# Kernel optimization log

Hardware: AMD Instinct MI355X
Metric: run time of the kernel (lower is better)

Reference implementation:

```python
import jax, jax.numpy as jnp
import numpy as np

EMBED_DIM = 1024
WINDOW = 256
NUM_HEADS = 16
HEAD_DIM = EMBED_DIM // NUM_HEADS
SCALE = HEAD_DIM ** (-0.5)


def setup_inputs() -> dict:
    key = jax.random.key(0)
    ks = jax.random.split(key, 9)
    B, S, E = 4, 4096, EMBED_DIM
    std = E ** (-0.5)
    x = jax.random.normal(ks[0], (B, S, E), dtype=jnp.float32)
    Wq = jax.random.normal(ks[1], (E, E), dtype=jnp.float32) * std
    Wk = jax.random.normal(ks[2], (E, E), dtype=jnp.float32) * std
    Wv = jax.random.normal(ks[3], (E, E), dtype=jnp.float32) * std
    Wo = jax.random.normal(ks[4], (E, E), dtype=jnp.float32) * std
    bq = jax.random.normal(ks[5], (E,), dtype=jnp.float32) * 0.01
    bk = jax.random.normal(ks[6], (E,), dtype=jnp.float32) * 0.01
    bv = jax.random.normal(ks[7], (E,), dtype=jnp.float32) * 0.01
    bo = jax.random.normal(ks[8], (E,), dtype=jnp.float32) * 0.01
    return {"x": x, "Wq": Wq, "bq": bq, "Wk": Wk, "bk": bk,
            "Wv": Wv, "bv": bv, "Wo": Wo, "bo": bo}


def reference(x, Wq, bq, Wk, bk, Wv, bv, Wo, bo):
    B, S, E = x.shape
    W = WINDOW
    nw = S // W  # seq_len chosen divisible by window_size
    # projections (torch Linear: x @ W.T + b); no head split in the original
    q = x @ Wq.T + bq
    k = x @ Wk.T + bk
    v = x @ Wv.T + bv
    # split into non-overlapping windows: [B, nw, W, E]
    qw = q.reshape(B, nw, W, E)
    kw = k.reshape(B, nw, W, E)
    vw = v.reshape(B, nw, W, E)
    scores = jnp.einsum('bnqe,bnke->bnqk', qw, kw) * SCALE  # [B, nw, W, W]
    causal = jnp.tril(jnp.ones((W, W), dtype=bool))
    scores = jnp.where(causal, scores, -jnp.inf)
    attn = jax.nn.softmax(scores, axis=-1)
    out = jnp.einsum('bnqk,bnke->bnqe', attn, vw).reshape(B, S, E)
    out = out @ Wo.T + bo
    return out + x
```

## Files before the change

### kernel.cpp

```cpp
#include <hip/hip_runtime.h>
#include <hip/hip_bf16.h>


typedef unsigned short u16;
typedef __attribute__((ext_vector_type(8))) short short8;
typedef __attribute__((ext_vector_type(4))) short short4v;
typedef __attribute__((ext_vector_type(4))) float f32x4;

__device__ __forceinline__ u16 f2bf(float f) {
    __hip_bfloat16 h = __float2bfloat16(f);
    return __builtin_bit_cast(u16, h);
}

__global__ void cast_f32_bf16(const float* __restrict__ src, u16* __restrict__ dst, int n) {
    int i = (blockIdx.x * 256 + threadIdx.x) * 8;
    if (i >= n) return;
    const float4* s = (const float4*)(src + i);
    float4 a = s[0], b = s[1];
    short8 o;
    o[0] = (short)f2bf(a.x); o[1] = (short)f2bf(a.y); o[2] = (short)f2bf(a.z); o[3] = (short)f2bf(a.w);
    o[4] = (short)f2bf(b.x); o[5] = (short)f2bf(b.y); o[6] = (short)f2bf(b.z); o[7] = (short)f2bf(b.w);
    *(short8*)(dst + i) = o;
}

__global__ void wcast(const float* __restrict__ Wq, const float* __restrict__ Wk,
                      const float* __restrict__ Wv, const float* __restrict__ Wo,
                      u16* __restrict__ WqT, u16* __restrict__ WkT,
                      u16* __restrict__ WvT, u16* __restrict__ Wob)
{
    __shared__ float lt[64][65];
    const int which = blockIdx.x >> 8;
    const int bid = blockIdx.x & 255;
    const int c0 = (bid & 15) * 64, r0 = (bid >> 4) * 64;
    const int t = threadIdx.x;
    const int tr = t >> 3, tc = (t & 7) * 8;
    const float* src = which == 0 ? Wq : which == 1 ? Wk : which == 2 ? Wv : Wo;
    if (which == 3) {
#pragma unroll
        for (int p = 0; p < 2; ++p) {
            int r = p * 32 + tr;
            const float* s = src + (size_t)(r0 + r) * 1024 + c0 + tc;
            float4 a = *(const float4*)s, b = *(const float4*)(s + 4);
            short8 o;
            o[0] = (short)f2bf(a.x); o[1] = (short)f2bf(a.y); o[2] = (short)f2bf(a.z); o[3] = (short)f2bf(a.w);
            o[4] = (short)f2bf(b.x); o[5] = (short)f2bf(b.y); o[6] = (short)f2bf(b.z); o[7] = (short)f2bf(b.w);
            *(short8*)(Wob + (size_t)(r0 + r) * 1024 + c0 + tc) = o;
        }
        return;
    }
    u16* dst = which == 0 ? WqT : which == 1 ? WkT : WvT;
#pragma unroll
    for (int p = 0; p < 2; ++p) {
        int r = p * 32 + tr;
        const float* s = src + (size_t)(r0 + r) * 1024 + c0 + tc;
        float4 a = *(const float4*)s, b = *(const float4*)(s + 4);
        lt[r][tc + 0] = a.x; lt[r][tc + 1] = a.y; lt[r][tc + 2] = a.z; lt[r][tc + 3] = a.w;
        lt[r][tc + 4] = b.x; lt[r][tc + 5] = b.y; lt[r][tc + 6] = b.z; lt[r][tc + 7] = b.w;
    }
    __syncthreads();
#pragma unroll
    for (int p = 0; p < 2; ++p) {
        int r = p * 32 + tr;
        short8 o;
#pragma unroll
        for (int j = 0; j < 8; ++j) o[j] = (short)f2bf(lt[tc + j][r]);
        *(short8*)(dst + (size_t)(c0 + r) * 1024 + r0 + tc) = o;
    }
}

__global__ void ub2(const float* __restrict__ Wk, const float* __restrict__ bq,
                    const float* __restrict__ Wo, const float* __restrict__ bv,
                    const float* __restrict__ bo, float* __restrict__ u, float* __restrict__ b2)
{
    const int t = threadIdx.x, bid = blockIdx.x;
    if (bid < 4) {
        int b = bid * 256 + t;
        float acc = 0.f;
        for (int o = 0; o < 1024; ++o) acc += Wk[(size_t)o * 1024 + b] * bq[o];
        u[b] = acc;
    } else {
        int n = (bid - 4) * 16 + (t >> 4);
        int l = t & 15;
        float acc = 0.f;
        for (int m = l; m < 1024; m += 16) acc += Wo[(size_t)n * 1024 + m] * bv[m];
#pragma unroll
        for (int s = 1; s < 16; s <<= 1) acc += __shfl_xor(acc, s, 64);
        if (l == 0) b2[n] = acc + bo[n];
    }
}

__global__ __launch_bounds__(256, 4) void gemm_small_dual(
    const u16* __restrict__ HA, const u16* __restrict__ HB, u16* __restrict__ HC,
    const u16* __restrict__ WA, const u16* __restrict__ WB, u16* __restrict__ WC)
{
    __shared__ __align__(16) u16 At[64 * 64], Bt[64 * 64];
    const bool sec = blockIdx.x >= 256;
    const u16* A = sec ? WA : HA;
    const u16* B = sec ? WB : HB;
    u16* C = sec ? WC : HC;
    const int bid = blockIdx.x & 255;
    const int m0 = (bid >> 4) * 64, n0 = (bid & 15) * 64;
    const int t = threadIdx.x, lane = t & 63, w = t >> 6;
    const int l15 = lane & 15, lk = lane >> 4;

    f32x4 acc[4];
#pragma unroll
    for (int m = 0; m < 4; ++m) acc[m] = (f32x4){0.f, 0.f, 0.f, 0.f};

    for (int k0 = 0; k0 < 1024; k0 += 64) {
        __syncthreads();
#pragma unroll
        for (int p = 0; p < 2; ++p) {
            int e = p * 2048 + t * 8;
            int row = e >> 6, col = e & 63;
            short8 va = *(const short8*)(A + (size_t)(m0 + row) * 1024 + k0 + col);
            *(short8*)((char*)At + row * 128 + ((col * 2) ^ ((row & 7) << 4))) = va;
            short8 vb = *(const short8*)(B + (size_t)(n0 + row) * 1024 + k0 + col);
            *(short8*)((char*)Bt + row * 128 + ((col * 2) ^ ((row & 7) << 4))) = vb;
        }
        __syncthreads();
#pragma unroll
        for (int ks = 0; ks < 2; ++ks) {
            int bc = ks * 64 + lk * 16;
            int brow = w * 16 + l15;
            short8 bfr = *(const short8*)((char*)Bt + brow * 128 + (bc ^ ((brow & 7) << 4)));
#pragma unroll
            for (int m = 0; m < 4; ++m) {
                int arow = m * 16 + l15;
                short8 af = *(const short8*)((char*)At + arow * 128 + (bc ^ ((arow & 7) << 4)));
                acc[m] = __builtin_amdgcn_mfma_f32_16x16x32_bf16(af, bfr, acc[m], 0, 0, 0);
            }
        }
    }
#pragma unroll
    for (int m = 0; m < 4; ++m)
#pragma unroll
        for (int r = 0; r < 4; ++r) {
            int row = m0 + m * 16 + lk * 4 + r;
            int col = n0 + w * 16 + l15;
            C[(size_t)row * 1024 + col] = f2bf(acc[m][r]);
        }
}

__global__ __launch_bounds__(256, 2) void gemm_yv(
    const u16* __restrict__ A, const u16* __restrict__ BH, const u16* __restrict__ BW,
    const float* __restrict__ ub, u16* __restrict__ Y, u16* __restrict__ V2t)
{
    __shared__ __align__(16) u16 At[128 * 64];
    __shared__ __align__(16) u16 Bt[128 * 64];
    const int t = threadIdx.x;
    const int lane = t & 63;
    const int wid = t >> 6;
    const int wm = wid >> 1, wn = wid & 1;
    const int l15 = lane & 15, lk = lane >> 4;
    const int K = 1024;

    const int bid = blockIdx.y * gridDim.x + blockIdx.x;
    const int cpx = 2048 >> 3;
    const int swz = (bid & 7) * cpx + (bid >> 3);
    const int tn = swz & 15;
    const int tm = swz >> 4;
    const int m0 = tm * 128;
    const bool isv = tn >= 8;
    const int n0 = (tn & 7) * 128;
    const u16* B = isv ? BW : BH;

    f32x4 acc[4][4];
#pragma unroll
    for (int m = 0; m < 4; ++m)
#pragma unroll
        for (int n = 0; n < 4; ++n)
            acc[m][n] = (f32x4){0.f, 0.f, 0.f, 0.f};

    for (int k0 = 0; k0 < K; k0 += 64) {
        __syncthreads();
#pragma unroll
        for (int p = 0; p < 4; ++p) {
            int e = p * 2048 + t * 8;
            int row = e >> 6, col = e & 63;
            short8 va = *(const short8*)(A + (size_t)(m0 + row) * K + k0 + col);
            *(short8*)((char*)At + row * 128 + ((col * 2) ^ ((row & 7) << 4))) = va;
            short8 vb = *(const short8*)(B + (size_t)(n0 + row) * K + k0 + col);
            *(short8*)((char*)Bt + row * 128 + ((col * 2) ^ ((row & 7) << 4))) = vb;
        }
        __syncthreads();
#pragma unroll
        for (int ks = 0; ks < 2; ++ks) {
            const int bc = ks * 64 + lk * 16;
            short8 af[4], bfr[4];
#pragma unroll
            for (int m = 0; m < 4; ++m) {
                int row = wm * 64 + m * 16 + l15;
                af[m] = *(const short8*)((char*)At + row * 128 + (bc ^ ((row & 7) << 4)));
            }
#pragma unroll
            for (int n = 0; n < 4; ++n) {
                int row = wn * 64 + n * 16 + l15;
                bfr[n] = *(const short8*)((char*)Bt + row * 128 + (bc ^ ((row & 7) << 4)));
            }
#pragma unroll
            for (int m = 0; m < 4; ++m)
#pragma unroll
                for (int n = 0; n < 4; ++n)
                    acc[m][n] = __builtin_amdgcn_mfma_f32_16x16x32_bf16(af[m], bfr[n], acc[m][n], 0, 0, 0);
        }
    }

    if (!isv) {
#pragma unroll
        for (int m = 0; m < 4; ++m)
#pragma unroll
            for (int n = 0; n < 4; ++n) {
                int col = n0 + wn * 64 + n * 16 + l15;
                float bv = ub[col];
#pragma unroll
                for (int r = 0; r < 4; ++r) {
                    int row = m0 + wm * 64 + m * 16 + lk * 4 + r;
                    Y[(size_t)row * 1024 + col] = f2bf(acc[m][n][r] + bv);
                }
            }
    } else {
#pragma unroll
        for (int m = 0; m < 4; ++m)
#pragma unroll
            for (int n = 0; n < 4; ++n) {
                int col = n0 + wn * 64 + n * 16 + l15;
                int row0 = m0 + wm * 64 + m * 16 + lk * 4;
                short4v pk;
#pragma unroll
                for (int r = 0; r < 4; ++r) pk[r] = (short)f2bf(acc[m][n][r]);
                *(short4v*)(V2t + (size_t)col * 16384 + row0) = pk;
            }
    }
}

__global__ __launch_bounds__(256, 2) void attn_win(
    const u16* __restrict__ y, const u16* __restrict__ xb,
    const u16* __restrict__ vt, const float* __restrict__ xres,
    const float* __restrict__ b2, float* __restrict__ outp)
{
    __shared__ __align__(16) char smem[75776];
    u16* Qt = (u16*)smem;
    u16* Kt = (u16*)(smem + 8192);
    u16* Vl = (u16*)smem;
    u16* P  = (u16*)(smem + 40960);
    float* rmax = (float*)(smem + 73728);
    float* rsum = (float*)(smem + 74752);

    const int t = threadIdx.x;
    const int lane = t & 63, wv = t >> 6;
    const int l15 = lane & 15, lk = lane >> 4;
    const int bid = blockIdx.x;
    const int swz = (bid & 7) * 32 + (bid >> 3);
    const int win = swz >> 2, qc = swz & 3;
    const size_t qrow0 = (size_t)win * 256 + qc * 64;
    const size_t krow0 = (size_t)win * 256;

    f32x4 acc[4][4];
#pragma unroll
    for (int m = 0; m < 4; ++m)
#pragma unroll
        for (int n = 0; n < 4; ++n)
            acc[m][n] = (f32x4){0.f, 0.f, 0.f, 0.f};

    for (int e0 = 0; e0 < 1024; e0 += 64) {
        __syncthreads();
#pragma unroll
        for (int p = 0; p < 2; ++p) {
            int e = p * 2048 + t * 8;
            int row = e >> 6, col = e & 63;
            short8 v = *(const short8*)(y + (qrow0 + row) * 1024 + e0 + col);
            *(short8*)((char*)Qt + row * 128 + ((col * 2) ^ ((row & 7) << 4))) = v;
        }
#pragma unroll
        for (int p = 0; p < 8; ++p) {
            int e = p * 2048 + t * 8;
            int row = e >> 6, col = e & 63;
            short8 v = *(const short8*)(xb + (krow0 + row) * 1024 + e0 + col);
            *(short8*)((char*)Kt + row * 128 + ((col * 2) ^ ((row & 7) << 4))) = v;
        }
        __syncthreads();
#pragma unroll
        for (int ks = 0; ks < 2; ++ks) {
            const int bc = ks * 64 + lk * 16;
            short8 af[4], bfr[4];
#pragma unroll
            for (int m = 0; m < 4; ++m) {
                int row = m * 16 + l15;
                af[m] = *(const short8*)((char*)Qt + row * 128 + (bc ^ ((row & 7) << 4)));
            }
#pragma unroll
            for (int n = 0; n < 4; ++n) {
                int row = wv * 64 + n * 16 + l15;
                bfr[n] = *(const short8*)((char*)Kt + row * 128 + (bc ^ ((row & 7) << 4)));
            }
            __builtin_amdgcn_s_setprio(1);
#pragma unroll
            for (int m = 0; m < 4; ++m)
#pragma unroll
                for (int n = 0; n < 4; ++n)
                    acc[m][n] = __builtin_amdgcn_mfma_f32_16x16x32_bf16(af[m], bfr[n], acc[m][n], 0, 0, 0);
            __builtin_amdgcn_s_setprio(0);
        }
    }

#pragma unroll
    for (int m = 0; m < 4; ++m)
#pragma unroll
        for (int n = 0; n < 4; ++n) {
            int col = wv * 64 + n * 16 + l15;
#pragma unroll
            for (int r = 0; r < 4; ++r) {
                int qpos = qc * 64 + m * 16 + lk * 4 + r;
                float v = acc[m][n][r] * 0.125f;
                acc[m][n][r] = (col <= qpos) ? v : -1e30f;
            }
        }
#pragma unroll
    for (int m = 0; m < 4; ++m)
#pragma unroll
        for (int r = 0; r < 4; ++r) {
            float tmx = fmaxf(fmaxf(acc[m][0][r], acc[m][1][r]), fmaxf(acc[m][2][r], acc[m][3][r]));
            tmx = fmaxf(tmx, __shfl_xor(tmx, 1));
            tmx = fmaxf(tmx, __shfl_xor(tmx, 2));
            tmx = fmaxf(tmx, __shfl_xor(tmx, 4));
            tmx = fmaxf(tmx, __shfl_xor(tmx, 8));
            if (l15 == 0) rmax[(m * 16 + lk * 4 + r) * 4 + wv] = tmx;
        }
    __syncthreads();
#pragma unroll
    for (int m = 0; m < 4; ++m)
#pragma unroll
        for (int r = 0; r < 4; ++r) {
            int row = m * 16 + lk * 4 + r;
            float m4 = fmaxf(fmaxf(rmax[row * 4], rmax[row * 4 + 1]),
                             fmaxf(rmax[row * 4 + 2], rmax[row * 4 + 3]));
            float s = 0.f;
#pragma unroll
            for (int n = 0; n < 4; ++n) {
                float e = __expf(acc[m][n][r] - m4);
                acc[m][n][r] = e;
                s += e;
            }
            s += __shfl_xor(s, 1);
            s += __shfl_xor(s, 2);
            s += __shfl_xor(s, 4);
            s += __shfl_xor(s, 8);
            if (l15 == 0) rsum[row * 4 + wv] = s;
        }
    __syncthreads();
#pragma unroll
    for (int m = 0; m < 4; ++m)
#pragma unroll
        for (int r = 0; r < 4; ++r) {
            int row = m * 16 + lk * 4 + r;
            float inv = 1.f / (rsum[row * 4] + rsum[row * 4 + 1] + rsum[row * 4 + 2] + rsum[row * 4 + 3]);
#pragma unroll
            for (int n = 0; n < 4; ++n) {
                int col = wv * 64 + n * 16 + l15;
                *(u16*)((char*)P + row * 512 + ((col * 2) ^ ((row & 7) << 4))) = f2bf(acc[m][n][r] * inv);
            }
        }

    for (int n0 = 0; n0 < 1024; n0 += 64) {
        __syncthreads();
#pragma unroll
        for (int p = 0; p < 8; ++p) {
            int e = p * 2048 + t * 8;
            int row = e >> 8, col = e & 255;
            short8 v = *(const short8*)(vt + (size_t)(n0 + row) * 16384 + win * 256 + col);
            *(short8*)((char*)Vl + row * 512 + ((col * 2) ^ ((row & 7) << 4))) = v;
        }
        __syncthreads();
        f32x4 acc2[4];
#pragma unroll
        for (int m = 0; m < 4; ++m) acc2[m] = (f32x4){0.f, 0.f, 0.f, 0.f};
#pragma unroll
        for (int ks = 0; ks < 8; ++ks) {
            const int bc = ks * 64 + lk * 16;
            short8 af[4];
#pragma unroll
            for (int m = 0; m < 4; ++m) {
                int row = m * 16 + l15;
                af[m] = *(const short8*)((char*)P + row * 512 + (bc ^ ((row & 7) << 4)));
            }
            int vrow = wv * 16 + l15;
            short8 bfr = *(const short8*)((char*)Vl + vrow * 512 + (bc ^ ((vrow & 7) << 4)));
            __builtin_amdgcn_s_setprio(1);
#pragma unroll
            for (int m = 0; m < 4; ++m)
                acc2[m] = __builtin_amdgcn_mfma_f32_16x16x32_bf16(af[m], bfr, acc2[m], 0, 0, 0);
            __builtin_amdgcn_s_setprio(0);
        }
#pragma unroll
        for (int m = 0; m < 4; ++m) {
#pragma unroll
            for (int r = 0; r < 4; ++r) {
                int row = m * 16 + lk * 4 + r;
                int col = n0 + wv * 16 + l15;
                size_t idx = (qrow0 + row) * 1024 + col;
                outp[idx] = acc2[m][r] + b2[col] + xres[idx];
            }
        }
    }
}

extern "C" void kernel_launch(void* const* d_in, const int* in_sizes, int n_in,
                              void* d_out, int out_size, void* d_ws, size_t ws_size,
                              hipStream_t stream) {
    const float* x  = (const float*)d_in[0];
    const float* Wq = (const float*)d_in[1];
    const float* bq = (const float*)d_in[2];
    const float* Wk = (const float*)d_in[3];
    const float* Wv = (const float*)d_in[5];
    const float* bv = (const float*)d_in[6];
    const float* Wo = (const float*)d_in[7];
    const float* bo = (const float*)d_in[8];
    float* out = (float*)d_out;

    char* ws = (char*)d_ws;
    u16* xb  = (u16*)(ws);
    u16* yb  = (u16*)(ws + 33554432);
    u16* v2t = (u16*)(ws + 67108864);
    u16* WqT = (u16*)(ws + 100663296);
    u16* WkT = (u16*)(ws + 102760448);
    u16* WvT = (u16*)(ws + 104857600);
    u16* Wob = (u16*)(ws + 106954752);
    u16* Hb  = (u16*)(ws + 109051904);
    u16* W2b = (u16*)(ws + 111149056);
    float* u_  = (float*)(ws + 113246208);
    float* b2_ = (float*)(ws + 113250304);

    cast_f32_bf16<<<8192, 256, 0, stream>>>(x, xb, 16777216);
    wcast<<<1024, 256, 0, stream>>>(Wq, Wk, Wv, Wo, WqT, WkT, WvT, Wob);
    ub2<<<68, 256, 0, stream>>>(Wk, bq, Wo, bv, bo, u_, b2_);
    gemm_small_dual<<<512, 256, 0, stream>>>(WkT, WqT, Hb, Wob, WvT, W2b);
    gemm_yv<<<dim3(16, 128), 256, 0, stream>>>(xb, Hb, W2b, u_, yb, v2t);
    attn_win<<<256, 256, 0, stream>>>(yb, xb, v2t, x, b2_, out);
}
```

Measured before the change: 207.6 us.

## Double-buffer Q/K and V tiles in LDS with register prefetch in attention kernel

```diff
diff --git a/kernel.cpp b/kernel.cpp
--- a/kernel.cpp
+++ b/kernel.cpp
@@ -234,18 +234,15 @@
     }
 }
 
-__global__ __launch_bounds__(256, 2) void attn_win(
+__global__ __launch_bounds__(256, 1) void attn_win(
     const u16* __restrict__ y, const u16* __restrict__ xb,
     const u16* __restrict__ vt, const float* __restrict__ xres,
     const float* __restrict__ b2, float* __restrict__ outp)
 {
-    __shared__ __align__(16) char smem[75776];
-    u16* Qt = (u16*)smem;
-    u16* Kt = (u16*)(smem + 8192);
-    u16* Vl = (u16*)smem;
-    u16* P  = (u16*)(smem + 40960);
-    float* rmax = (float*)(smem + 73728);
-    float* rsum = (float*)(smem + 74752);
+    __shared__ __align__(16) char smem[116736];
+    u16* P  = (u16*)(smem + 81920);
+    float* rmax = (float*)(smem + 114688);
+    float* rsum = (float*)(smem + 115712);
 
     const int t = threadIdx.x;
     const int lane = t & 63, wv = t >> 6;
@@ -263,23 +260,49 @@
         for (int n = 0; n < 4; ++n)
             acc[m][n] = (f32x4){0.f, 0.f, 0.f, 0.f};
 
-    for (int e0 = 0; e0 < 1024; e0 += 64) {
-        __syncthreads();
+    short8 pq[2], pk[8];
+    auto LOAD_QK = [&](int e0) {
 #pragma unroll
         for (int p = 0; p < 2; ++p) {
             int e = p * 2048 + t * 8;
+            pq[p] = *(const short8*)(y + (qrow0 + (e >> 6)) * 1024 + e0 + (e & 63));
+        }
+#pragma unroll
+        for (int p = 0; p < 8; ++p) {
+            int e = p * 2048 + t * 8;
+            pk[p] = *(const short8*)(xb + (krow0 + (e >> 6)) * 1024 + e0 + (e & 63));
+        }
+    };
+    auto WRITE_QK = [&](int b) {
+        char* Qt = smem + b * 40960;
+        char* Kt = Qt + 8192;
+#pragma unroll
+        for (int p = 0; p < 2; ++p) {
+            int e = p * 2048 + t * 8;
             int row = e >> 6, col = e & 63;
-            short8 v = *(const short8*)(y + (qrow0 + row) * 1024 + e0 + col);
-            *(short8*)((char*)Qt + row * 128 + ((col * 2) ^ ((row & 7) << 4))) = v;
+            *(short8*)(Qt + row * 128 + ((col * 2) ^ ((row & 7) << 4))) = pq[p];
         }
 #pragma unroll
         for (int p = 0; p < 8; ++p) {
             int e = p * 2048 + t * 8;
             int row = e >> 6, col = e & 63;
-            short8 v = *(const short8*)(xb + (krow0 + row) * 1024 + e0 + col);
-            *(short8*)((char*)Kt + row * 128 + ((col * 2) ^ ((row & 7) << 4))) = v;
-        }
-        __syncthreads();
+            *(short8*)(Kt + row * 128 + ((col * 2) ^ ((row & 7) << 4))) = pk[p];
+        }
+    };
+
+    LOAD_QK(0);
+    WRITE_QK(0);
+    LOAD_QK(64);
+    __syncthreads();
+
+    for (int i = 0; i < 16; ++i) {
+        const int b = i & 1;
+        if (i + 1 < 16) {
+            WRITE_QK(b ^ 1);
+            if (i + 2 < 16) LOAD_QK((i + 2) * 64);
+        }
+        const char* Qt = smem + b * 40960;
+        const char* Kt = Qt + 8192;
 #pragma unroll
         for (int ks = 0; ks < 2; ++ks) {
             const int bc = ks * 64 + lk * 16;
@@ -287,12 +310,12 @@
 #pragma unroll
             for (int m = 0; m < 4; ++m) {
                 int row = m * 16 + l15;
-                af[m] = *(const short8*)((char*)Qt + row * 128 + (bc ^ ((row & 7) << 4)));
+                af[m] = *(const short8*)(Qt + row * 128 + (bc ^ ((row & 7) << 4)));
             }
 #pragma unroll
             for (int n = 0; n < 4; ++n) {
                 int row = wv * 64 + n * 16 + l15;
-                bfr[n] = *(const short8*)((char*)Kt + row * 128 + (bc ^ ((row & 7) << 4)));
+                bfr[n] = *(const short8*)(Kt + row * 128 + (bc ^ ((row & 7) << 4)));
             }
             __builtin_amdgcn_s_setprio(1);
 #pragma unroll
@@ -302,6 +325,7 @@
                     acc[m][n] = __builtin_amdgcn_mfma_f32_16x16x32_bf16(af[m], bfr[n], acc[m][n], 0, 0, 0);
             __builtin_amdgcn_s_setprio(0);
         }
+        __syncthreads();
     }
 
 #pragma unroll
@@ -362,16 +386,37 @@
             }
         }
 
-    for (int n0 = 0; n0 < 1024; n0 += 64) {
-        __syncthreads();
+    short8 pv[8];
+    auto LOAD_V = [&](int n0) {
 #pragma unroll
         for (int p = 0; p < 8; ++p) {
             int e = p * 2048 + t * 8;
+            pv[p] = *(const short8*)(vt + (size_t)(n0 + (e >> 8)) * 16384 + win * 256 + (e & 255));
+        }
+    };
+    auto WRITE_V = [&](int b) {
+        char* Vl = smem + b * 40960;
+#pragma unroll
+        for (int p = 0; p < 8; ++p) {
+            int e = p * 2048 + t * 8;
             int row = e >> 8, col = e & 255;
-            short8 v = *(const short8*)(vt + (size_t)(n0 + row) * 16384 + win * 256 + col);
-            *(short8*)((char*)Vl + row * 512 + ((col * 2) ^ ((row & 7) << 4))) = v;
-        }
-        __syncthreads();
+            *(short8*)(Vl + row * 512 + ((col * 2) ^ ((row & 7) << 4))) = pv[p];
+        }
+    };
+
+    LOAD_V(0);
+    WRITE_V(0);
+    LOAD_V(64);
+    __syncthreads();
+
+    for (int i = 0; i < 16; ++i) {
+        const int b = i & 1;
+        const int n0 = i * 64;
+        if (i + 1 < 16) {
+            WRITE_V(b ^ 1);
+            if (i + 2 < 16) LOAD_V((i + 2) * 64);
+        }
+        const char* Vl = smem + b * 40960;
         f32x4 acc2[4];
 #pragma unroll
         for (int m = 0; m < 4; ++m) acc2[m] = (f32x4){0.f, 0.f, 0.f, 0.f};
@@ -385,7 +430,7 @@
                 af[m] = *(const short8*)((char*)P + row * 512 + (bc ^ ((row & 7) << 4)));
             }
             int vrow = wv * 16 + l15;
-            short8 bfr = *(const short8*)((char*)Vl + vrow * 512 + (bc ^ ((vrow & 7) << 4)));
+            short8 bfr = *(const short8*)(Vl + vrow * 512 + (bc ^ ((vrow & 7) << 4)));
             __builtin_amdgcn_s_setprio(1);
 #pragma unroll
             for (int m = 0; m < 4; ++m)
@@ -402,6 +447,7 @@
                 outp[idx] = acc2[m][r] + b2[col] + xres[idx];
             }
         }
+        __syncthreads();
     }
 }
 
```

New measurement: 198.2 us. 4.5% less time.
